# Performance work log

Hardware: AMD Instinct MI355X
Metric: run time of the kernel (lower is better)

The kernel has to match this reference:

```python
import jax, jax.numpy as jnp
import numpy as np

B, L, D = 32, 2048, 768
H = 512
EPS = 1e-5  # batch_norm eps (PyG MLP default norm)


def setup_inputs() -> dict:
    key = jax.random.key(0)
    ks = jax.random.split(key, 8)
    hidden = jax.random.normal(ks[0], (B, L, D), dtype=jnp.float32)
    attention_mask = jax.random.randint(ks[1], (B, L), 0, 2, dtype=jnp.int32)
    W1 = jax.random.normal(ks[2], (D, H), dtype=jnp.float32) * 0.02
    b1 = jnp.zeros((H,), dtype=jnp.float32)
    gamma = jnp.ones((H,), dtype=jnp.float32)
    beta = jnp.zeros((H,), dtype=jnp.float32)
    W2 = jax.random.normal(ks[3], (H, H), dtype=jnp.float32) * 0.02
    b2 = jnp.zeros((H,), dtype=jnp.float32)
    return {"hidden": hidden, "attention_mask": attention_mask,
            "W1": W1, "b1": b1, "gamma": gamma, "beta": beta,
            "W2": W2, "b2": b2}


def reference(hidden, attention_mask, W1, b1, gamma, beta, W2, b2):
    # Valid-token mask; pads are excluded from the batched graph's node set.
    m = attention_mask.astype(hidden.dtype)[..., None]  # (B, L, 1)
    n_valid = jnp.maximum(jnp.sum(m), 1.0)

    # MLP layer 1: Linear -> BatchNorm (stats over all valid nodes across the
    # whole batched graph, mirroring PyG MLP training-mode batch_norm) -> ReLU
    h = jnp.einsum('bld,dh->blh', hidden, W1) + b1  # (B, L, H)
    mean = jnp.sum(h * m, axis=(0, 1)) / n_valid
    var = jnp.sum(jnp.square(h - mean) * m, axis=(0, 1)) / n_valid
    h = (h - mean) * jax.lax.rsqrt(var + EPS) * gamma + beta
    h = jax.nn.relu(h)

    # MLP layer 2 (plain_last: no norm/act)
    out = jnp.einsum('blh,hk->blk', h, W2) + b2  # (B, L, H)

    # scores == ones -> segment softmax over each sequence's valid tokens is
    # uniform 1/n_b; scatter_add over batch ids == masked mean pool.
    counts = jnp.maximum(jnp.sum(m, axis=1), 1.0)  # (B, 1)
    pooled = jnp.sum(out * m, axis=1) / counts  # (B, H)
    return pooled
```

## Files before the change

kernel.cpp:

```cpp
#include <hip/hip_runtime.h>
#include <hip/hip_bf16.h>

#define Bn 32
#define Ln 2048
#define Dn 768
#define Hn 512
#define Mn (Bn*Ln)
#define EPSC 1e-5f

#define OFF_S1   0
#define OFF_S2   512
#define OFF_CNT  2048
#define OFF_PH   2304
#define OFF_W1T_BYTES  131072
#define OFF_H_BYTES    1048576

#define BM 128
#define BN2 256
#define BK 64
#define LDK 72

typedef __attribute__((ext_vector_type(8))) short bf16x8;
typedef __attribute__((ext_vector_type(4))) float f32x4;

static __device__ __forceinline__ unsigned short f2bf(float x) {
  __hip_bfloat16 h = __float2bfloat16(x);
  return *reinterpret_cast<unsigned short*>(&h);
}
static __device__ __forceinline__ float bf2f(unsigned short u) {
  return __uint_as_float(((unsigned int)u) << 16);
}

__global__ __launch_bounds__(256) void pre_kernel(const int* __restrict__ mask,
                                                  float* __restrict__ ws) {
  int blk = blockIdx.x, t = threadIdx.x;
  if (blk < Bn) {
    __shared__ int red[256];
    int s = 0;
#pragma unroll
    for (int i = 0; i < 8; i++) s += mask[blk * Ln + i * 256 + t];
    red[t] = s;
    __syncthreads();
    for (int off = 128; off > 0; off >>= 1) {
      if (t < off) red[t] += red[t + off];
      __syncthreads();
    }
    if (t == 0) ws[OFF_CNT + blk] = (float)red[0];
  } else {
#pragma unroll
    for (int i = 0; i < 4; i++) ws[OFF_S1 + i * 256 + t] = 0.f;
#pragma unroll
    for (int i = 0; i < 64; i++) ws[OFF_PH + i * 256 + t] = 0.f;
  }
}

__global__ __launch_bounds__(256) void transpose_w1(
    const float* __restrict__ W1, unsigned short* __restrict__ W1t) {
  __shared__ float tile[32][33];
  int kx = blockIdx.x * 32;
  int nx = blockIdx.y * 32;
  int tx = threadIdx.x & 31, ty = threadIdx.x >> 5;
#pragma unroll
  for (int i = 0; i < 32; i += 8)
    tile[ty + i][tx] = W1[(size_t)(kx + ty + i) * Hn + nx + tx];
  __syncthreads();
#pragma unroll
  for (int i = 0; i < 32; i += 8)
    W1t[(size_t)(nx + ty + i) * Dn + kx + tx] = f2bf(tile[tx][ty + i]);
}

__global__ __launch_bounds__(512, 4) void gemm1_mfma(
    const float* __restrict__ A, const unsigned short* __restrict__ W1t,
    const float* __restrict__ b1, const int* __restrict__ mask,
    unsigned short* __restrict__ Hout,
    float* __restrict__ gsum, float* __restrict__ gsq)
{
  __shared__ unsigned short As[BM * LDK];
  __shared__ unsigned short Bs[BN2 * LDK];
  __shared__ float csum[BN2];
  __shared__ float csq[BN2];

  const int t = threadIdx.x;
  const int bx = blockIdx.x;
  const int by = blockIdx.y;
  const int bm0 = by * BM;
  const int bn0 = bx * BN2;

  const int w = t >> 6;
  const int lane = t & 63;
  const int wm0 = (w >> 2) * 64;
  const int wn0 = (w & 3) * 64;
  const int l15 = lane & 15;
  const int quad = lane >> 4;

  const int am = t >> 2;
  const int ak = (t & 3) * 16;
  const int bn = t >> 1;
  const int bk = (t & 1) * 32;

  const float* Ap = A + (size_t)(bm0 + am) * Dn + ak;
  const unsigned short* Bp = W1t + (size_t)(bn0 + bn) * Dn + bk;

  f32x4 acc[4][4];
#pragma unroll
  for (int i = 0; i < 4; i++)
#pragma unroll
    for (int j = 0; j < 4; j++) acc[i][j] = (f32x4){0.f, 0.f, 0.f, 0.f};

  for (int k0 = 0; k0 < Dn; k0 += BK) {
    float4 a0 = *(const float4*)(Ap + k0);
    float4 a1 = *(const float4*)(Ap + k0 + 4);
    float4 a2 = *(const float4*)(Ap + k0 + 8);
    float4 a3 = *(const float4*)(Ap + k0 + 12);
    uint4 bv0 = *(const uint4*)(Bp + k0);
    uint4 bv1 = *(const uint4*)(Bp + k0 + 8);
    uint4 bv2 = *(const uint4*)(Bp + k0 + 16);
    uint4 bv3 = *(const uint4*)(Bp + k0 + 24);
    __syncthreads();
    uint4 p0, p1;
    p0.x = (unsigned int)f2bf(a0.x) | ((unsigned int)f2bf(a0.y) << 16);
    p0.y = (unsigned int)f2bf(a0.z) | ((unsigned int)f2bf(a0.w) << 16);
    p0.z = (unsigned int)f2bf(a1.x) | ((unsigned int)f2bf(a1.y) << 16);
    p0.w = (unsigned int)f2bf(a1.z) | ((unsigned int)f2bf(a1.w) << 16);
    p1.x = (unsigned int)f2bf(a2.x) | ((unsigned int)f2bf(a2.y) << 16);
    p1.y = (unsigned int)f2bf(a2.z) | ((unsigned int)f2bf(a2.w) << 16);
    p1.z = (unsigned int)f2bf(a3.x) | ((unsigned int)f2bf(a3.y) << 16);
    p1.w = (unsigned int)f2bf(a3.z) | ((unsigned int)f2bf(a3.w) << 16);
    *(uint4*)&As[am * LDK + ak] = p0;
    *(uint4*)&As[am * LDK + ak + 8] = p1;
    *(uint4*)&Bs[bn * LDK + bk] = bv0;
    *(uint4*)&Bs[bn * LDK + bk + 8] = bv1;
    *(uint4*)&Bs[bn * LDK + bk + 16] = bv2;
    *(uint4*)&Bs[bn * LDK + bk + 24] = bv3;
    __syncthreads();
#pragma unroll
    for (int s = 0; s < 2; s++) {
      bf16x8 af[4], bf[4];
#pragma unroll
      for (int mt = 0; mt < 4; mt++)
        af[mt] = *(const bf16x8*)&As[(wm0 + mt * 16 + l15) * LDK + s * 32 + quad * 8];
#pragma unroll
      for (int nt = 0; nt < 4; nt++)
        bf[nt] = *(const bf16x8*)&Bs[(wn0 + nt * 16 + l15) * LDK + s * 32 + quad * 8];
#pragma unroll
      for (int mt = 0; mt < 4; mt++)
#pragma unroll
        for (int nt = 0; nt < 4; nt++)
          acc[mt][nt] = __builtin_amdgcn_mfma_f32_16x16x32_bf16(
              af[mt], bf[nt], acc[mt][nt], 0, 0, 0);
    }
  }

  if (t < BN2) { csum[t] = 0.f; csq[t] = 0.f; }
  __syncthreads();

  float mk[4][4];
#pragma unroll
  for (int mt = 0; mt < 4; mt++) {
    int4 mv = *(const int4*)(mask + bm0 + wm0 + mt * 16 + quad * 4);
    mk[mt][0] = (float)mv.x; mk[mt][1] = (float)mv.y;
    mk[mt][2] = (float)mv.z; mk[mt][3] = (float)mv.w;
  }

  const size_t cbase = ((size_t)(by * 2 + bx)) * 32768 + (size_t)w * 4096;
#pragma unroll
  for (int nt = 0; nt < 4; nt++) {
    const int nl = wn0 + nt * 16 + l15;
    const float bias = b1[bn0 + nl];
    float ps = 0.f, pq = 0.f;
#pragma unroll
    for (int mt = 0; mt < 4; mt++) {
      ushort4 st;
      float v0 = acc[mt][nt][0] + bias;
      float v1 = acc[mt][nt][1] + bias;
      float v2 = acc[mt][nt][2] + bias;
      float v3 = acc[mt][nt][3] + bias;
      ps += v0 * mk[mt][0] + v1 * mk[mt][1] + v2 * mk[mt][2] + v3 * mk[mt][3];
      pq += v0 * v0 * mk[mt][0] + v1 * v1 * mk[mt][1] +
            v2 * v2 * mk[mt][2] + v3 * v3 * mk[mt][3];
      st.x = f2bf(v0); st.y = f2bf(v1); st.z = f2bf(v2); st.w = f2bf(v3);
      *(ushort4*)&Hout[cbase + (size_t)(mt * 4 + nt) * 256 + lane * 4] = st;
    }
    atomicAdd(&csum[nl], ps);
    atomicAdd(&csq[nl], pq);
  }

  __syncthreads();
  if (t < BN2) {
    atomicAdd(&gsum[bn0 + t], csum[t]);
    atomicAdd(&gsq[bn0 + t], csq[t]);
  }
}

__global__ __launch_bounds__(256) void bnpool_kernel(
    const unsigned short* __restrict__ Hbuf, const int* __restrict__ mask,
    const float* __restrict__ ws, const float* __restrict__ gamma,
    const float* __restrict__ beta, float* __restrict__ PH)
{
  __shared__ float mkf[BM];
  __shared__ float redc[32];
  const int t = threadIdx.x;
  const int chunk = blockIdx.x;
  const int by = chunk >> 1, bx = chunk & 1;
  const int b = chunk >> 5;
  if (t < 32) redc[t] = ws[OFF_CNT + t];
  if (t < BM) mkf[t] = (float)mask[by * BM + t];
  __syncthreads();

  float nv = 0.f;
#pragma unroll
  for (int i = 0; i < 32; i++) nv += redc[i];
  nv = fmaxf(nv, 1.f);
  const float inv = 1.f / nv;
  const int c = bx * BN2 + t;
  const float m = ws[OFF_S1 + c] * inv;
  const float var = ws[OFF_S2 + c] * inv - m * m;
  const float istd = rsqrtf(fmaxf(var, 0.f) + EPSC);
  const float scv = istd * gamma[c];
  const float shv = beta[c] - m * scv;

  const int w3 = t >> 6, nt = (t >> 4) & 3, l15 = t & 15;
  float acc = 0.f;
#pragma unroll
  for (int h = 0; h < 2; h++) {
    const int w = w3 + h * 4;
    const int wm0 = h * 64;
    const unsigned short* base =
        Hbuf + (size_t)chunk * 32768 + (size_t)w * 4096 + nt * 256 + l15 * 4;
#pragma unroll
    for (int mt = 0; mt < 4; mt++)
#pragma unroll
      for (int q = 0; q < 4; q++) {
        ushort4 hv = *(const ushort4*)(base + mt * 1024 + q * 64);
        const float* mv = &mkf[wm0 + mt * 16 + q * 4];
        acc += fmaxf(fmaf(bf2f(hv.x), scv, shv), 0.f) * mv[0]
             + fmaxf(fmaf(bf2f(hv.y), scv, shv), 0.f) * mv[1]
             + fmaxf(fmaf(bf2f(hv.z), scv, shv), 0.f) * mv[2]
             + fmaxf(fmaf(bf2f(hv.w), scv, shv), 0.f) * mv[3];
      }
  }
  atomicAdd(&PH[b * Hn + c], acc);
}

__global__ __launch_bounds__(128) void final_kernel(
    const float* __restrict__ pooledh, const float* __restrict__ cnt,
    const float* __restrict__ W2, const float* __restrict__ b2,
    float* __restrict__ out)
{
  __shared__ float pr[Hn];
  int b = blockIdx.x >> 2;
  int cc = blockIdx.x & 3;
  int t = threadIdx.x;
  float nb = cnt[b];
  float inv = 1.f / fmaxf(nb, 1.f);
#pragma unroll
  for (int i = 0; i < 4; i++)
    pr[t + i * 128] = pooledh[b * Hn + t + i * 128] * inv;
  __syncthreads();
  int c = cc * 128 + t;
  float a0 = 0.f, a1 = 0.f, a2 = 0.f, a3 = 0.f;
  for (int i = 0; i < Hn; i += 4) {
    a0 = fmaf(pr[i],     W2[(size_t)i * Hn + c],       a0);
    a1 = fmaf(pr[i + 1], W2[(size_t)(i + 1) * Hn + c], a1);
    a2 = fmaf(pr[i + 2], W2[(size_t)(i + 2) * Hn + c], a2);
    a3 = fmaf(pr[i + 3], W2[(size_t)(i + 3) * Hn + c], a3);
  }
  out[b * Hn + c] = (a0 + a1) + (a2 + a3) + b2[c] * (nb * inv);
}

extern "C" void kernel_launch(void* const* d_in, const int* in_sizes, int n_in,
                              void* d_out, int out_size, void* d_ws, size_t ws_size,
                              hipStream_t stream) {
  const float* hidden = (const float*)d_in[0];
  const int*   mask   = (const int*)d_in[1];
  const float* W1     = (const float*)d_in[2];
  const float* b1     = (const float*)d_in[3];
  const float* gamma  = (const float*)d_in[4];
  const float* beta   = (const float*)d_in[5];
  const float* W2     = (const float*)d_in[6];
  const float* b2     = (const float*)d_in[7];
  float* out = (float*)d_out;
  float* ws  = (float*)d_ws;
  unsigned short* W1t  = (unsigned short*)((char*)d_ws + OFF_W1T_BYTES);
  unsigned short* Hbuf = (unsigned short*)((char*)d_ws + OFF_H_BYTES);

  pre_kernel<<<Bn + 1, 256, 0, stream>>>(mask, ws);
  transpose_w1<<<dim3(Dn / 32, Hn / 32), 256, 0, stream>>>(W1, W1t);
  gemm1_mfma<<<dim3(Hn / BN2, Mn / BM), 512, 0, stream>>>(
      hidden, W1t, b1, mask, Hbuf, ws + OFF_S1, ws + OFF_S2);
  bnpool_kernel<<<(Mn / BM) * (Hn / BN2), 256, 0, stream>>>(
      Hbuf, mask, ws, gamma, beta, ws + OFF_PH);
  final_kernel<<<Bn * 4, 128, 0, stream>>>(ws + OFF_PH, ws + OFF_CNT, W2, b2, out);
}
```

Baseline: 390.2 us.

## Triple-buffer GEMM1 with direct global-to-LDS B loads and swizzled LDS

Rewrites the first GEMM main loop as a hand-scheduled, triple-buffered pipeline. The W1t tile is fetched straight into LDS with global_load_lds, and the activation tile is prefetched two k-steps ahead in registers, converted to bf16 and stored one step ahead. Padded LDS rows are replaced by an XOR swizzle, and explicit waitcnt/barrier/setprio calls let MFMA work overlap the next tile's loads. The W1 transpose is also merged into the prep kernel to save one launch. This raises LDS use and removes the occupancy hint, which may lower waves per CU.

```diff
diff --git a/kernel.cpp b/kernel.cpp
--- a/kernel.cpp
+++ b/kernel.cpp
@@ -18,7 +18,7 @@
 #define BM 128
 #define BN2 256
 #define BK 64
-#define LDK 72
+#define KT_N 12
 
 typedef __attribute__((ext_vector_type(8))) short bf16x8;
 typedef __attribute__((ext_vector_type(4))) float f32x4;
@@ -31,8 +31,9 @@
   return __uint_as_float(((unsigned int)u) << 16);
 }
 
-__global__ __launch_bounds__(256) void pre_kernel(const int* __restrict__ mask,
-                                                  float* __restrict__ ws) {
+__global__ __launch_bounds__(256) void prep_kernel(
+    const int* __restrict__ mask, const float* __restrict__ W1,
+    unsigned short* __restrict__ W1t, float* __restrict__ ws) {
   int blk = blockIdx.x, t = threadIdx.x;
   if (blk < Bn) {
     __shared__ int red[256];
@@ -46,39 +47,35 @@
       __syncthreads();
     }
     if (t == 0) ws[OFF_CNT + blk] = (float)red[0];
+  } else if (blk == Bn) {
+#pragma unroll
+    for (int i = 0; i < 4; i++) ws[OFF_S1 + i * 256 + t] = 0.f;
+#pragma unroll
+    for (int i = 0; i < 64; i++) ws[OFF_PH + i * 256 + t] = 0.f;
   } else {
-#pragma unroll
-    for (int i = 0; i < 4; i++) ws[OFF_S1 + i * 256 + t] = 0.f;
-#pragma unroll
-    for (int i = 0; i < 64; i++) ws[OFF_PH + i * 256 + t] = 0.f;
-  }
-}
-
-__global__ __launch_bounds__(256) void transpose_w1(
-    const float* __restrict__ W1, unsigned short* __restrict__ W1t) {
-  __shared__ float tile[32][33];
-  int kx = blockIdx.x * 32;
-  int nx = blockIdx.y * 32;
-  int tx = threadIdx.x & 31, ty = threadIdx.x >> 5;
-#pragma unroll
-  for (int i = 0; i < 32; i += 8)
-    tile[ty + i][tx] = W1[(size_t)(kx + ty + i) * Hn + nx + tx];
-  __syncthreads();
-#pragma unroll
-  for (int i = 0; i < 32; i += 8)
-    W1t[(size_t)(nx + ty + i) * Dn + kx + tx] = f2bf(tile[tx][ty + i]);
-}
-
-__global__ __launch_bounds__(512, 4) void gemm1_mfma(
+    __shared__ float tile[32][33];
+    int tb = blk - (Bn + 1);
+    int kx = (tb % 24) * 32;
+    int nx = (tb / 24) * 32;
+    int tx = t & 31, ty = t >> 5;
+#pragma unroll
+    for (int i = 0; i < 32; i += 8)
+      tile[ty + i][tx] = W1[(size_t)(kx + ty + i) * Hn + nx + tx];
+    __syncthreads();
+#pragma unroll
+    for (int i = 0; i < 32; i += 8)
+      W1t[(size_t)(nx + ty + i) * Dn + kx + tx] = f2bf(tile[tx][ty + i]);
+  }
+}
+
+__global__ __launch_bounds__(512) void gemm1_mfma(
     const float* __restrict__ A, const unsigned short* __restrict__ W1t,
     const float* __restrict__ b1, const int* __restrict__ mask,
     unsigned short* __restrict__ Hout,
     float* __restrict__ gsum, float* __restrict__ gsq)
 {
-  __shared__ unsigned short As[BM * LDK];
-  __shared__ unsigned short Bs[BN2 * LDK];
-  __shared__ float csum[BN2];
-  __shared__ float csq[BN2];
+  __shared__ __align__(16) unsigned short As3[3][BM * BK];
+  __shared__ __align__(16) unsigned short Bs3[3][BN2 * BK];
 
   const int t = threadIdx.x;
   const int bx = blockIdx.x;
@@ -92,14 +89,26 @@
   const int wn0 = (w & 3) * 64;
   const int l15 = lane & 15;
   const int quad = lane >> 4;
+  const int swz = (l15 & 7) << 4;
+  const int aAr = (wm0 + l15) * 128;
+  const int aBr = (wn0 + l15) * 128;
 
   const int am = t >> 2;
-  const int ak = (t & 3) * 16;
-  const int bn = t >> 1;
-  const int bk = (t & 1) * 32;
-
-  const float* Ap = A + (size_t)(bm0 + am) * Dn + ak;
-  const unsigned short* Bp = W1t + (size_t)(bn0 + bn) * Dn + bk;
+  const int akc = (t & 3) * 16;
+  const float* Ap = A + (size_t)(bm0 + am) * Dn + akc;
+  const int ab0 = am * 128 + ((akc * 2) ^ ((am & 7) << 4));
+  const int ab1 = am * 128 + ((akc * 2 + 16) ^ ((am & 7) << 4));
+
+  const int p0 = ((w * 2 + 0) << 10) + (lane << 4);
+  const int p1 = ((w * 2 + 1) << 10) + (lane << 4);
+  const int q0 = p0 ^ (((p0 >> 7) & 7) << 4);
+  const int q1 = p1 ^ (((p1 >> 7) & 7) << 4);
+  const char* bsrc00 = (const char*)(W1t + (size_t)(bn0 +   0 + (q0 >> 7)) * Dn) + (q0 & 127);
+  const char* bsrc01 = (const char*)(W1t + (size_t)(bn0 +   0 + (q1 >> 7)) * Dn) + (q1 & 127);
+  const char* bsrc10 = (const char*)(W1t + (size_t)(bn0 + 128 + (q0 >> 7)) * Dn) + (q0 & 127);
+  const char* bsrc11 = (const char*)(W1t + (size_t)(bn0 + 128 + (q1 >> 7)) * Dn) + (q1 & 127);
+  const int bd0 = (w * 2 + 0) << 10;
+  const int bd1 = (w * 2 + 1) << 10;
 
   f32x4 acc[4][4];
 #pragma unroll
@@ -107,50 +116,125 @@
 #pragma unroll
     for (int j = 0; j < 4; j++) acc[i][j] = (f32x4){0.f, 0.f, 0.f, 0.f};
 
-  for (int k0 = 0; k0 < Dn; k0 += BK) {
-    float4 a0 = *(const float4*)(Ap + k0);
-    float4 a1 = *(const float4*)(Ap + k0 + 4);
-    float4 a2 = *(const float4*)(Ap + k0 + 8);
-    float4 a3 = *(const float4*)(Ap + k0 + 12);
-    uint4 bv0 = *(const uint4*)(Bp + k0);
-    uint4 bv1 = *(const uint4*)(Bp + k0 + 8);
-    uint4 bv2 = *(const uint4*)(Bp + k0 + 16);
-    uint4 bv3 = *(const uint4*)(Bp + k0 + 24);
-    __syncthreads();
-    uint4 p0, p1;
-    p0.x = (unsigned int)f2bf(a0.x) | ((unsigned int)f2bf(a0.y) << 16);
-    p0.y = (unsigned int)f2bf(a0.z) | ((unsigned int)f2bf(a0.w) << 16);
-    p0.z = (unsigned int)f2bf(a1.x) | ((unsigned int)f2bf(a1.y) << 16);
-    p0.w = (unsigned int)f2bf(a1.z) | ((unsigned int)f2bf(a1.w) << 16);
-    p1.x = (unsigned int)f2bf(a2.x) | ((unsigned int)f2bf(a2.y) << 16);
-    p1.y = (unsigned int)f2bf(a2.z) | ((unsigned int)f2bf(a2.w) << 16);
-    p1.z = (unsigned int)f2bf(a3.x) | ((unsigned int)f2bf(a3.y) << 16);
-    p1.w = (unsigned int)f2bf(a3.z) | ((unsigned int)f2bf(a3.w) << 16);
-    *(uint4*)&As[am * LDK + ak] = p0;
-    *(uint4*)&As[am * LDK + ak + 8] = p1;
-    *(uint4*)&Bs[bn * LDK + bk] = bv0;
-    *(uint4*)&Bs[bn * LDK + bk + 8] = bv1;
-    *(uint4*)&Bs[bn * LDK + bk + 16] = bv2;
-    *(uint4*)&Bs[bn * LDK + bk + 24] = bv3;
-    __syncthreads();
-#pragma unroll
-    for (int s = 0; s < 2; s++) {
-      bf16x8 af[4], bf[4];
-#pragma unroll
-      for (int mt = 0; mt < 4; mt++)
-        af[mt] = *(const bf16x8*)&As[(wm0 + mt * 16 + l15) * LDK + s * 32 + quad * 8];
-#pragma unroll
-      for (int nt = 0; nt < 4; nt++)
-        bf[nt] = *(const bf16x8*)&Bs[(wn0 + nt * 16 + l15) * LDK + s * 32 + quad * 8];
-#pragma unroll
-      for (int mt = 0; mt < 4; mt++)
-#pragma unroll
-        for (int nt = 0; nt < 4; nt++)
-          acc[mt][nt] = __builtin_amdgcn_mfma_f32_16x16x32_bf16(
-              af[mt], bf[nt], acc[mt][nt], 0, 0, 0);
-    }
-  }
-
+  float4 rAe[4], rAo[4];
+  bf16x8 af0, af1, af2, af3, bf0, bf1, bf2, bf3;
+
+#define WAITV(N) do { asm volatile("s_waitcnt vmcnt(" #N ")" ::: "memory"); \
+                      __builtin_amdgcn_sched_barrier(0); } while (0)
+#define LG0()    do { asm volatile("s_waitcnt lgkmcnt(0)" ::: "memory"); \
+                      __builtin_amdgcn_sched_barrier(0); } while (0)
+
+#define SBH(KT, H) do { \
+  __builtin_amdgcn_global_load_lds( \
+      (const __attribute__((address_space(1))) void*)(((H) ? bsrc10 : bsrc00) + (KT) * 128), \
+      (__attribute__((address_space(3))) void*)((char*)&Bs3[(KT) % 3][0] + (H) * 16384 + bd0), \
+      16, 0, 0); \
+  __builtin_amdgcn_global_load_lds( \
+      (const __attribute__((address_space(1))) void*)(((H) ? bsrc11 : bsrc01) + (KT) * 128), \
+      (__attribute__((address_space(3))) void*)((char*)&Bs3[(KT) % 3][0] + (H) * 16384 + bd1), \
+      16, 0, 0); \
+} while (0)
+
+#define AG(KT2, R) do { \
+  R[0] = *(const float4*)(Ap + (KT2) * BK); \
+  R[1] = *(const float4*)(Ap + (KT2) * BK + 4); \
+  R[2] = *(const float4*)(Ap + (KT2) * BK + 8); \
+  R[3] = *(const float4*)(Ap + (KT2) * BK + 12); \
+} while (0)
+
+#define WRA(R, KTD) do { \
+  uint4 w0, w1; \
+  w0.x = (unsigned)f2bf(R[0].x) | ((unsigned)f2bf(R[0].y) << 16); \
+  w0.y = (unsigned)f2bf(R[0].z) | ((unsigned)f2bf(R[0].w) << 16); \
+  w0.z = (unsigned)f2bf(R[1].x) | ((unsigned)f2bf(R[1].y) << 16); \
+  w0.w = (unsigned)f2bf(R[1].z) | ((unsigned)f2bf(R[1].w) << 16); \
+  w1.x = (unsigned)f2bf(R[2].x) | ((unsigned)f2bf(R[2].y) << 16); \
+  w1.y = (unsigned)f2bf(R[2].z) | ((unsigned)f2bf(R[2].w) << 16); \
+  w1.z = (unsigned)f2bf(R[3].x) | ((unsigned)f2bf(R[3].y) << 16); \
+  w1.w = (unsigned)f2bf(R[3].z) | ((unsigned)f2bf(R[3].w) << 16); \
+  *(uint4*)((char*)&As3[(KTD) % 3][0] + ab0) = w0; \
+  *(uint4*)((char*)&As3[(KTD) % 3][0] + ab1) = w1; \
+} while (0)
+
+#define DSR(KT, S) do { \
+  const char* Ab = (const char*)&As3[(KT) % 3][0]; \
+  const char* Bb = (const char*)&Bs3[(KT) % 3][0]; \
+  const int co = ((S) * 64 + quad * 16) ^ swz; \
+  af0 = *(const bf16x8*)(Ab + aAr +    0 + co); \
+  af1 = *(const bf16x8*)(Ab + aAr + 2048 + co); \
+  af2 = *(const bf16x8*)(Ab + aAr + 4096 + co); \
+  af3 = *(const bf16x8*)(Ab + aAr + 6144 + co); \
+  bf0 = *(const bf16x8*)(Bb + aBr +    0 + co); \
+  bf1 = *(const bf16x8*)(Bb + aBr + 2048 + co); \
+  bf2 = *(const bf16x8*)(Bb + aBr + 4096 + co); \
+  bf3 = *(const bf16x8*)(Bb + aBr + 6144 + co); \
+} while (0)
+
+#define MFMAS() do { \
+  acc[0][0] = __builtin_amdgcn_mfma_f32_16x16x32_bf16(af0, bf0, acc[0][0], 0, 0, 0); \
+  acc[0][1] = __builtin_amdgcn_mfma_f32_16x16x32_bf16(af0, bf1, acc[0][1], 0, 0, 0); \
+  acc[0][2] = __builtin_amdgcn_mfma_f32_16x16x32_bf16(af0, bf2, acc[0][2], 0, 0, 0); \
+  acc[0][3] = __builtin_amdgcn_mfma_f32_16x16x32_bf16(af0, bf3, acc[0][3], 0, 0, 0); \
+  acc[1][0] = __builtin_amdgcn_mfma_f32_16x16x32_bf16(af1, bf0, acc[1][0], 0, 0, 0); \
+  acc[1][1] = __builtin_amdgcn_mfma_f32_16x16x32_bf16(af1, bf1, acc[1][1], 0, 0, 0); \
+  acc[1][2] = __builtin_amdgcn_mfma_f32_16x16x32_bf16(af1, bf2, acc[1][2], 0, 0, 0); \
+  acc[1][3] = __builtin_amdgcn_mfma_f32_16x16x32_bf16(af1, bf3, acc[1][3], 0, 0, 0); \
+  acc[2][0] = __builtin_amdgcn_mfma_f32_16x16x32_bf16(af2, bf0, acc[2][0], 0, 0, 0); \
+  acc[2][1] = __builtin_amdgcn_mfma_f32_16x16x32_bf16(af2, bf1, acc[2][1], 0, 0, 0); \
+  acc[2][2] = __builtin_amdgcn_mfma_f32_16x16x32_bf16(af2, bf2, acc[2][2], 0, 0, 0); \
+  acc[2][3] = __builtin_amdgcn_mfma_f32_16x16x32_bf16(af2, bf3, acc[2][3], 0, 0, 0); \
+  acc[3][0] = __builtin_amdgcn_mfma_f32_16x16x32_bf16(af3, bf0, acc[3][0], 0, 0, 0); \
+  acc[3][1] = __builtin_amdgcn_mfma_f32_16x16x32_bf16(af3, bf1, acc[3][1], 0, 0, 0); \
+  acc[3][2] = __builtin_amdgcn_mfma_f32_16x16x32_bf16(af3, bf2, acc[3][2], 0, 0, 0); \
+  acc[3][3] = __builtin_amdgcn_mfma_f32_16x16x32_bf16(af3, bf3, acc[3][3], 0, 0, 0); \
+} while (0)
+
+#define KTB(KT, RAG, RWR) do { \
+   \
+  if ((KT) < 11) { WAITV(8); } else { WAITV(0); } \
+  DSR(KT, 0); \
+  if ((KT) <= 9) AG((KT) + 2, RAG); \
+  if ((KT) >= 1 && (KT) <= 10) WRA(RWR, (KT) + 1); \
+  if ((KT) <= 9) SBH((KT) + 2, 0); \
+  __builtin_amdgcn_s_barrier(); \
+  LG0(); \
+  __builtin_amdgcn_s_setprio(1); MFMAS(); __builtin_amdgcn_s_setprio(0); \
+  __builtin_amdgcn_s_barrier(); \
+   \
+  DSR(KT, 1); \
+  if ((KT) <= 9) SBH((KT) + 2, 1); \
+  __builtin_amdgcn_s_barrier(); \
+  LG0(); \
+  __builtin_amdgcn_s_setprio(1); MFMAS(); __builtin_amdgcn_s_setprio(0); \
+  __builtin_amdgcn_s_barrier(); \
+} while (0)
+
+  AG(0, rAe);
+  WRA(rAe, 0);
+  AG(1, rAo);
+  WRA(rAo, 1);
+  SBH(0, 0); SBH(0, 1); SBH(1, 0); SBH(1, 1);
+  WAITV(4);
+  LG0();
+  __builtin_amdgcn_s_barrier();
+
+#pragma unroll
+  for (int k2 = 0; k2 < 6; ++k2) {
+    KTB(k2 * 2,     rAe, rAo);
+    KTB(k2 * 2 + 1, rAo, rAe);
+  }
+
+#undef KTB
+#undef MFMAS
+#undef DSR
+#undef WRA
+#undef AG
+#undef SBH
+#undef LG0
+#undef WAITV
+
+  float* csum = (float*)&As3[0][0];
+  float* csq  = csum + BN2;
   if (t < BN2) { csum[t] = 0.f; csq[t] = 0.f; }
   __syncthreads();
 
@@ -284,8 +368,8 @@
   unsigned short* W1t  = (unsigned short*)((char*)d_ws + OFF_W1T_BYTES);
   unsigned short* Hbuf = (unsigned short*)((char*)d_ws + OFF_H_BYTES);
 
-  pre_kernel<<<Bn + 1, 256, 0, stream>>>(mask, ws);
-  transpose_w1<<<dim3(Dn / 32, Hn / 32), 256, 0, stream>>>(W1, W1t);
+  prep_kernel<<<Bn + 1 + (Dn / 32) * (Hn / 32), 256, 0, stream>>>(
+      mask, W1, W1t, ws);
   gemm1_mfma<<<dim3(Hn / BN2, Mn / BM), 512, 0, stream>>>(
       hidden, W1t, b1, mask, Hbuf, ws + OFF_S1, ws + OFF_S2);
   bnpool_kernel<<<(Mn / BM) * (Hn / BN2), 256, 0, stream>>>(
```

After: 406.3 us. 1.04x slower.

## Load W1 tile directly to LDS with XOR swizzle and merge prep kernels

Applied to the files above, without the earlier changes.

The GEMM1 B operand now goes straight from global memory into LDS through global_load_lds, bypassing registers. The LDS tile is unpadded and uses an XOR swizzle to avoid bank conflicts, and the MFMA fragment reads apply the matching swizzle. The mask count, workspace zeroing and W1 transpose kernels are merged into one launch to save launch overhead. The swizzle address math and the direct-to-LDS path are subtle, and a mistake would corrupt results.

```diff
diff --git a/kernel.cpp b/kernel.cpp
--- a/kernel.cpp
+++ b/kernel.cpp
@@ -19,6 +19,7 @@
 #define BN2 256
 #define BK 64
 #define LDK 72
+#define KT_N (Dn/BK)
 
 typedef __attribute__((ext_vector_type(8))) short bf16x8;
 typedef __attribute__((ext_vector_type(4))) float f32x4;
@@ -31,8 +32,9 @@
   return __uint_as_float(((unsigned int)u) << 16);
 }
 
-__global__ __launch_bounds__(256) void pre_kernel(const int* __restrict__ mask,
-                                                  float* __restrict__ ws) {
+__global__ __launch_bounds__(256) void prep_kernel(
+    const int* __restrict__ mask, const float* __restrict__ W1,
+    unsigned short* __restrict__ W1t, float* __restrict__ ws) {
   int blk = blockIdx.x, t = threadIdx.x;
   if (blk < Bn) {
     __shared__ int red[256];
@@ -46,27 +48,25 @@
       __syncthreads();
     }
     if (t == 0) ws[OFF_CNT + blk] = (float)red[0];
+  } else if (blk == Bn) {
+#pragma unroll
+    for (int i = 0; i < 4; i++) ws[OFF_S1 + i * 256 + t] = 0.f;
+#pragma unroll
+    for (int i = 0; i < 64; i++) ws[OFF_PH + i * 256 + t] = 0.f;
   } else {
-#pragma unroll
-    for (int i = 0; i < 4; i++) ws[OFF_S1 + i * 256 + t] = 0.f;
-#pragma unroll
-    for (int i = 0; i < 64; i++) ws[OFF_PH + i * 256 + t] = 0.f;
-  }
-}
-
-__global__ __launch_bounds__(256) void transpose_w1(
-    const float* __restrict__ W1, unsigned short* __restrict__ W1t) {
-  __shared__ float tile[32][33];
-  int kx = blockIdx.x * 32;
-  int nx = blockIdx.y * 32;
-  int tx = threadIdx.x & 31, ty = threadIdx.x >> 5;
-#pragma unroll
-  for (int i = 0; i < 32; i += 8)
-    tile[ty + i][tx] = W1[(size_t)(kx + ty + i) * Hn + nx + tx];
-  __syncthreads();
-#pragma unroll
-  for (int i = 0; i < 32; i += 8)
-    W1t[(size_t)(nx + ty + i) * Dn + kx + tx] = f2bf(tile[tx][ty + i]);
+    __shared__ float tile[32][33];
+    int tb = blk - (Bn + 1);
+    int kx = (tb % 24) * 32;
+    int nx = (tb / 24) * 32;
+    int tx = t & 31, ty = t >> 5;
+#pragma unroll
+    for (int i = 0; i < 32; i += 8)
+      tile[ty + i][tx] = W1[(size_t)(kx + ty + i) * Hn + nx + tx];
+    __syncthreads();
+#pragma unroll
+    for (int i = 0; i < 32; i += 8)
+      W1t[(size_t)(nx + ty + i) * Dn + kx + tx] = f2bf(tile[tx][ty + i]);
+  }
 }
 
 __global__ __launch_bounds__(512, 4) void gemm1_mfma(
@@ -76,7 +76,7 @@
     float* __restrict__ gsum, float* __restrict__ gsq)
 {
   __shared__ unsigned short As[BM * LDK];
-  __shared__ unsigned short Bs[BN2 * LDK];
+  __shared__ __align__(16) unsigned short Bs[BN2 * BK];
   __shared__ float csum[BN2];
   __shared__ float csq[BN2];
 
@@ -95,11 +95,20 @@
 
   const int am = t >> 2;
   const int ak = (t & 3) * 16;
-  const int bn = t >> 1;
-  const int bk = (t & 1) * 32;
-
   const float* Ap = A + (size_t)(bm0 + am) * Dn + ak;
-  const unsigned short* Bp = W1t + (size_t)(bn0 + bn) * Dn + bk;
+
+  const int p0 = ((w * 4 + 0) << 10) + (lane << 4);
+  const int p1 = ((w * 4 + 1) << 10) + (lane << 4);
+  const int p2 = ((w * 4 + 2) << 10) + (lane << 4);
+  const int p3 = ((w * 4 + 3) << 10) + (lane << 4);
+  const int q0 = p0 ^ (((p0 >> 7) & 7) << 4);
+  const int q1 = p1 ^ (((p1 >> 7) & 7) << 4);
+  const int q2 = p2 ^ (((p2 >> 7) & 7) << 4);
+  const int q3 = p3 ^ (((p3 >> 7) & 7) << 4);
+  const char* bsrc0 = (const char*)(W1t + (size_t)(bn0 + (q0 >> 7)) * Dn) + (q0 & 127);
+  const char* bsrc1 = (const char*)(W1t + (size_t)(bn0 + (q1 >> 7)) * Dn) + (q1 & 127);
+  const char* bsrc2 = (const char*)(W1t + (size_t)(bn0 + (q2 >> 7)) * Dn) + (q2 & 127);
+  const char* bsrc3 = (const char*)(W1t + (size_t)(bn0 + (q3 >> 7)) * Dn) + (q3 & 127);
 
   f32x4 acc[4][4];
 #pragma unroll
@@ -112,26 +121,34 @@
     float4 a1 = *(const float4*)(Ap + k0 + 4);
     float4 a2 = *(const float4*)(Ap + k0 + 8);
     float4 a3 = *(const float4*)(Ap + k0 + 12);
-    uint4 bv0 = *(const uint4*)(Bp + k0);
-    uint4 bv1 = *(const uint4*)(Bp + k0 + 8);
-    uint4 bv2 = *(const uint4*)(Bp + k0 + 16);
-    uint4 bv3 = *(const uint4*)(Bp + k0 + 24);
     __syncthreads();
-    uint4 p0, p1;
-    p0.x = (unsigned int)f2bf(a0.x) | ((unsigned int)f2bf(a0.y) << 16);
-    p0.y = (unsigned int)f2bf(a0.z) | ((unsigned int)f2bf(a0.w) << 16);
-    p0.z = (unsigned int)f2bf(a1.x) | ((unsigned int)f2bf(a1.y) << 16);
-    p0.w = (unsigned int)f2bf(a1.z) | ((unsigned int)f2bf(a1.w) << 16);
-    p1.x = (unsigned int)f2bf(a2.x) | ((unsigned int)f2bf(a2.y) << 16);
-    p1.y = (unsigned int)f2bf(a2.z) | ((unsigned int)f2bf(a2.w) << 16);
-    p1.z = (unsigned int)f2bf(a3.x) | ((unsigned int)f2bf(a3.y) << 16);
-    p1.w = (unsigned int)f2bf(a3.z) | ((unsigned int)f2bf(a3.w) << 16);
-    *(uint4*)&As[am * LDK + ak] = p0;
-    *(uint4*)&As[am * LDK + ak + 8] = p1;
-    *(uint4*)&Bs[bn * LDK + bk] = bv0;
-    *(uint4*)&Bs[bn * LDK + bk + 8] = bv1;
-    *(uint4*)&Bs[bn * LDK + bk + 16] = bv2;
-    *(uint4*)&Bs[bn * LDK + bk + 24] = bv3;
+    __builtin_amdgcn_global_load_lds(
+        (const __attribute__((address_space(1))) void*)(bsrc0 + k0 * 2),
+        (__attribute__((address_space(3))) void*)((char*)&Bs[0] + ((w * 4 + 0) << 10)),
+        16, 0, 0);
+    __builtin_amdgcn_global_load_lds(
+        (const __attribute__((address_space(1))) void*)(bsrc1 + k0 * 2),
+        (__attribute__((address_space(3))) void*)((char*)&Bs[0] + ((w * 4 + 1) << 10)),
+        16, 0, 0);
+    __builtin_amdgcn_global_load_lds(
+        (const __attribute__((address_space(1))) void*)(bsrc2 + k0 * 2),
+        (__attribute__((address_space(3))) void*)((char*)&Bs[0] + ((w * 4 + 2) << 10)),
+        16, 0, 0);
+    __builtin_amdgcn_global_load_lds(
+        (const __attribute__((address_space(1))) void*)(bsrc3 + k0 * 2),
+        (__attribute__((address_space(3))) void*)((char*)&Bs[0] + ((w * 4 + 3) << 10)),
+        16, 0, 0);
+    uint4 w0, w1;
+    w0.x = (unsigned)f2bf(a0.x) | ((unsigned)f2bf(a0.y) << 16);
+    w0.y = (unsigned)f2bf(a0.z) | ((unsigned)f2bf(a0.w) << 16);
+    w0.z = (unsigned)f2bf(a1.x) | ((unsigned)f2bf(a1.y) << 16);
+    w0.w = (unsigned)f2bf(a1.z) | ((unsigned)f2bf(a1.w) << 16);
+    w1.x = (unsigned)f2bf(a2.x) | ((unsigned)f2bf(a2.y) << 16);
+    w1.y = (unsigned)f2bf(a2.z) | ((unsigned)f2bf(a2.w) << 16);
+    w1.z = (unsigned)f2bf(a3.x) | ((unsigned)f2bf(a3.y) << 16);
+    w1.w = (unsigned)f2bf(a3.z) | ((unsigned)f2bf(a3.w) << 16);
+    *(uint4*)&As[am * LDK + ak] = w0;
+    *(uint4*)&As[am * LDK + ak + 8] = w1;
     __syncthreads();
 #pragma unroll
     for (int s = 0; s < 2; s++) {
@@ -140,8 +157,11 @@
       for (int mt = 0; mt < 4; mt++)
         af[mt] = *(const bf16x8*)&As[(wm0 + mt * 16 + l15) * LDK + s * 32 + quad * 8];
 #pragma unroll
-      for (int nt = 0; nt < 4; nt++)
-        bf[nt] = *(const bf16x8*)&Bs[(wn0 + nt * 16 + l15) * LDK + s * 32 + quad * 8];
+      for (int nt = 0; nt < 4; nt++) {
+        const int rb = wn0 + nt * 16 + l15;
+        const int cb = (s * 64 + quad * 16) ^ ((rb & 7) << 4);
+        bf[nt] = *(const bf16x8*)((const char*)&Bs[0] + rb * 128 + cb);
+      }
 #pragma unroll
       for (int mt = 0; mt < 4; mt++)
 #pragma unroll
@@ -284,8 +304,8 @@
   unsigned short* W1t  = (unsigned short*)((char*)d_ws + OFF_W1T_BYTES);
   unsigned short* Hbuf = (unsigned short*)((char*)d_ws + OFF_H_BYTES);
 
-  pre_kernel<<<Bn + 1, 256, 0, stream>>>(mask, ws);
-  transpose_w1<<<dim3(Dn / 32, Hn / 32), 256, 0, stream>>>(W1, W1t);
+  prep_kernel<<<Bn + 1 + (Dn / 32) * (Hn / 32), 256, 0, stream>>>(
+      mask, W1, W1t, ws);
   gemm1_mfma<<<dim3(Hn / BN2, Mn / BM), 512, 0, stream>>>(
       hidden, W1t, b1, mask, Hbuf, ws + OFF_S1, ws + OFF_S2);
   bnpool_kernel<<<(Mn / BM) * (Hn / BN2), 256, 0, stream>>>(
```

Result: faster. 368.8 us (-5.5%).
